# Kernel tuning notes

Measured on AMD Instinct MI355X. Metric: run time of the kernel, lower is better.

## Reference

```python
import jax, jax.numpy as jnp
import numpy as np

EPS = 1e-9
NEG_BIG = -(2.0**32) + 1.0


def dice(x, alpha):
    # BN with center=False, scale=False at inference: moving_mean=0, moving_var=1
    x_norm = x * (1.0 / np.sqrt(1.0 + EPS)).astype(np.float32)
    p = jax.nn.sigmoid(x_norm)
    return alpha * (1.0 - p) * x + p * x


def setup_inputs() -> dict:
    key = jax.random.key(0)
    ks = jax.random.split(key, 12)
    B, T, D = 4096, 200, 128
    U = 128  # gru units == hidden_dim

    def glorot(k, shape):
        fan_in = shape[0]
        return (jax.random.normal(k, shape, dtype=jnp.float32) / np.sqrt(fan_in)).astype(jnp.float32)

    return {
        "interest_seq": jax.random.normal(ks[0], (B, T, D), dtype=jnp.float32),
        "target_emb": jax.random.normal(ks[1], (B, D), dtype=jnp.float32),
        "seq_length": jax.random.randint(ks[2], (B, 1), 0, T, dtype=jnp.int32),
        "W_att1": glorot(ks[3], (4 * D, 64)),
        "alpha1": jnp.zeros((64,), jnp.float32),
        "W_att2": glorot(ks[4], (64, 16)),
        "alpha2": jnp.zeros((16,), jnp.float32),
        "W_att3": glorot(ks[5], (16, 1)),
        "W_u": glorot(ks[6], (D + U, U)),
        "W_r": glorot(ks[7], (D + U, U)),
        "W_c": glorot(ks[8], (D + U, U)),
    }


def reference(interest_seq, target_emb, seq_length, W_att1, alpha1, W_att2, alpha2, W_att3, W_u, W_r, W_c):
    B, T, D = interest_seq.shape
    U = W_u.shape[1]

    # ---- Attention scores (return_score=True, sigmoid, no weight norm) ----
    q = jnp.broadcast_to(target_emb[:, None, :], (B, T, D))  # [B,T,D]
    k = interest_seq
    att_in = jnp.concatenate([q, k, q - k, q * k], axis=-1)  # [B,T,4D]
    h1 = dice(jnp.einsum('btf,fh->bth', att_in, W_att1), alpha1)
    h2 = dice(jnp.einsum('bth,hg->btg', h1, W_att2), alpha2)
    score = jnp.einsum('btg,go->bto', h2, W_att3)  # [B,T,1]

    valid = jnp.arange(T)[None, :] < seq_length  # [B,T] bool
    vmask = valid.astype(jnp.float32)[:, :, None]
    score = score * vmask + (1.0 - vmask) * NEG_BIG
    att = jax.nn.sigmoid(score)[:, :, 0]  # [B,T]

    # ---- AUGRU scan (return final hidden state) ----
    def step(h, xs):
        x_t, a_t, m_t = xs  # [B,D], [B], [B] bool
        gi = jnp.concatenate([x_t, h], axis=-1)  # [B, D+U]
        u = jax.nn.sigmoid(gi @ W_u)
        r = jax.nn.sigmoid(gi @ W_r)
        c = jnp.tanh(jnp.concatenate([x_t, r * h], axis=-1) @ W_c)
        u_t = u * a_t[:, None]
        h_new = (1.0 - u_t) * h + u_t * c
        h = jnp.where(m_t[:, None], h_new, h)
        return h, None

    xs = (jnp.swapaxes(interest_seq, 0, 1),  # [T,B,D]
          att.T,                              # [T,B]
          valid.T)                            # [T,B]
    h0 = jnp.zeros((B, U), dtype=interest_seq.dtype)
    h_final, _ = jax.lax.scan(step, h0, xs)
    return h_final
```

## Files before the change

kernel.cpp:

```cpp
#include <hip/hip_runtime.h>
#include <math.h>

typedef __bf16 bf16;
typedef __bf16 bf16x8 __attribute__((ext_vector_type(8)));
typedef float  f32x4  __attribute__((ext_vector_type(4)));

#define MFMA16(a,b,c) __builtin_amdgcn_mfma_f32_16x16x32_bf16((a),(b),(c),0,0,0)

#define B_SZ 4096
#define T_SZ 200
#define D_SZ 128
#define U_SZ 128
#define ACHUNK 4
#define AROWS 16
#define ATTB 8

__device__ __forceinline__ float frcp_(float x) { return __builtin_amdgcn_rcpf(x); }
__device__ __forceinline__ float fsig(float x)  { return frcp_(1.0f + __expf(-x)); }
__device__ __forceinline__ float ftanh_(float x){ return 1.0f - 2.0f * frcp_(1.0f + __expf(2.0f * x)); }
__device__ __forceinline__ float dicef(float x, float alpha) {
    float p = fsig(x);
    return alpha * (1.0f - p) * x + p * x;
}
__device__ __forceinline__ void bar_lgkm() {
    asm volatile("s_waitcnt lgkmcnt(0)\n\ts_barrier" ::: "memory");
}

__global__ __launch_bounds__(256) void prep_kernel(
    const float* __restrict__ Q,
    const float* __restrict__ W1,
    const float* __restrict__ W2,
    float* __restrict__ BIAS,
    bf16*  __restrict__ W1P,
    bf16*  __restrict__ W2T)
{
    const int tid = threadIdx.x;
    if (blockIdx.x == 256) {
        #pragma unroll 4
        for (int it = 0; it < 64; ++it) {
            int idx = it * 256 + tid;
            int k = idx >> 6;
            int n = idx & 63;
            float v;
            if (k < 128) v = W1[(128 + k) * 64 + n] - W1[(256 + k) * 64 + n];
            else         v = W1[(384 + (k - 128)) * 64 + n];
            W1P[n * 256 + k] = (bf16)v;
        }
        #pragma unroll
        for (int it = 0; it < 4; ++it) {
            int idx = it * 256 + tid; int k = idx >> 4; int n = idx & 15;
            W2T[n * 64 + k] = (bf16)W2[k * 16 + n];
        }
        return;
    }
    const int b0   = blockIdx.x * 16;
    const int lane = tid & 63;
    const int w    = tid >> 6;
    const int quad = lane >> 4;
    const int l15  = lane & 15;

    bf16x8 a[4];
    #pragma unroll
    for (int kk = 0; kk < 4; ++kk) {
        const float* p = Q + (long)(b0 + l15) * D_SZ + kk * 32 + quad * 8;
        float4 x0 = ((const float4*)p)[0];
        float4 x1 = ((const float4*)p)[1];
        float xv[8] = {x0.x, x0.y, x0.z, x0.w, x1.x, x1.y, x1.z, x1.w};
        #pragma unroll
        for (int j = 0; j < 8; ++j) a[kk][j] = (bf16)xv[j];
    }
    const int n = w * 16 + l15;
    f32x4 acc = {};
    #pragma unroll
    for (int kk = 0; kk < 4; ++kk) {
        bf16x8 bf;
        #pragma unroll
        for (int j = 0; j < 8; ++j) {
            int k = kk * 32 + quad * 8 + j;
            bf[j] = (bf16)(W1[k * 64 + n] + W1[(256 + k) * 64 + n]);
        }
        acc = MFMA16(a[kk], bf, acc);
    }
    #pragma unroll
    for (int i = 0; i < 4; ++i)
        BIAS[(long)(b0 + quad * 4 + i) * 64 + n] = acc[i];
}

__global__ __launch_bounds__(256) void attn_kernel(
    const float* __restrict__ X,
    const float* __restrict__ Q,
    const int*   __restrict__ LEN,
    const float* __restrict__ A1,
    const float* __restrict__ A2,
    const float* __restrict__ W3,
    const float* __restrict__ BIAS,
    const bf16*  __restrict__ W1P,
    const bf16*  __restrict__ W2T,
    float* __restrict__ ATT)
{
    __shared__ bf16  H1s[64][72];
    __shared__ float qf[ATTB][128];
    __shared__ float bias_s[ATTB][64];
    __shared__ float al1[64];
    __shared__ float al2[16];
    __shared__ float w3s[16];
    __shared__ int   lens[ATTB];

    const int tid  = threadIdx.x;
    const int lane = tid & 63;
    const int w    = tid >> 6;
    const int quad = lane >> 4;
    const int l15  = lane & 15;
    const long b0  = (long)blockIdx.x * ATTB;

    for (int i = tid; i < ATTB * 128; i += 256) qf[i >> 7][i & 127] = Q[b0 * 128 + i];
    for (int i = tid; i < ATTB * 64;  i += 256) bias_s[i >> 6][i & 63] = BIAS[b0 * 64 + i];
    if (tid < 64) al1[tid] = A1[tid];
    if (tid < 16) { al2[tid] = A2[tid]; w3s[tid] = W3[tid]; }
    if (tid < ATTB) lens[tid] = LEN[b0 + tid];

    bf16x8 b1[4][8];
    #pragma unroll
    for (int nt = 0; nt < 4; ++nt)
        #pragma unroll
        for (int kk = 0; kk < 8; ++kk)
            b1[nt][kk] = *(const bf16x8*)(W1P + (nt * 16 + l15) * 256 + kk * 32 + quad * 8);
    bf16x8 b2[2];
    #pragma unroll
    for (int kk = 0; kk < 2; ++kk)
        b2[kk] = *(const bf16x8*)(W2T + l15 * 64 + kk * 32 + quad * 8);
    __syncthreads();

    const int NT = 13 * ATTB;
    float4 fb[8];
    auto issue = [&](int g) {
        int bi = g / 13, mt = g - bi * 13;
        int row = mt * 16 + l15;
        int rc  = row < T_SZ ? row : (T_SZ - 1);
        const float* xp = X + ((b0 + bi) * T_SZ + rc) * D_SZ;
        #pragma unroll
        for (int kc = 0; kc < 4; ++kc) {
            const float* p = xp + kc * 32 + quad * 8;
            fb[kc * 2]     = ((const float4*)p)[0];
            fb[kc * 2 + 1] = ((const float4*)p)[1];
        }
    };
    auto convert = [&](int g, bf16x8* axd, bf16x8* aqd) {
        int bi = g / 13;
        #pragma unroll
        for (int kc = 0; kc < 4; ++kc) {
            float4 xa = fb[kc * 2], xb = fb[kc * 2 + 1];
            float xv[8] = {xa.x, xa.y, xa.z, xa.w, xb.x, xb.y, xb.z, xb.w};
            const float* qp = &qf[bi][kc * 32 + quad * 8];
            #pragma unroll
            for (int j = 0; j < 8; ++j) {
                axd[kc][j] = (bf16)xv[j];
                aqd[kc][j] = (bf16)(xv[j] * qp[j]);
            }
        }
    };

    bf16x8 axc[4], aqc[4];
    issue(w);
    convert(w, axc, aqc);

    for (int g = w; g < NT; g += 4) {
        const int gn = g + 4;
        if (gn < NT) issue(gn);

        f32x4 acc[4] = {};
        #pragma unroll
        for (int kc = 0; kc < 4; ++kc)
            #pragma unroll
            for (int nt = 0; nt < 4; ++nt) {
                acc[nt] = MFMA16(axc[kc], b1[nt][kc],     acc[nt]);
                acc[nt] = MFMA16(aqc[kc], b1[nt][kc + 4], acc[nt]);
            }

        const int bi = g / 13, mt = g - bi * 13;
        const int m0 = mt * 16;
        #pragma unroll
        for (int nt = 0; nt < 4; ++nt) {
            int n = nt * 16 + l15;
            float bia = bias_s[bi][n]; float al = al1[n];
            #pragma unroll
            for (int i = 0; i < 4; ++i) {
                float v = acc[nt][i] + bia;
                H1s[w * 16 + quad * 4 + i][n] = (bf16)dicef(v, al);
            }
        }
        f32x4 acc2 = {};
        #pragma unroll
        for (int kk = 0; kk < 2; ++kk) {
            bf16x8 a2 = *(const bf16x8*)&H1s[w * 16 + l15][kk * 32 + quad * 8];
            acc2 = MFMA16(a2, b2[kk], acc2);
        }
        {
            float al = al2[l15]; float w3 = w3s[l15];
            float s[4];
            #pragma unroll
            for (int i = 0; i < 4; ++i) s[i] = dicef(acc2[i], al) * w3;
            #pragma unroll
            for (int i = 0; i < 4; ++i) {
                s[i] += __shfl_xor(s[i], 1, 64);
                s[i] += __shfl_xor(s[i], 2, 64);
                s[i] += __shfl_xor(s[i], 4, 64);
                s[i] += __shfl_xor(s[i], 8, 64);
            }
            if (l15 == 0) {
                int len = lens[bi];
                #pragma unroll
                for (int i = 0; i < 4; ++i) {
                    int t = m0 + quad * 4 + i;
                    if (t < T_SZ)
                        ATT[(b0 + bi) * T_SZ + t] = (t < len) ? fsig(s[i]) : 0.0f;
                }
            }
        }
        if (gn < NT) convert(gn, axc, aqc);
    }
}

__global__ __launch_bounds__(512) void augru_kernel(
    const float* __restrict__ X,
    const float* __restrict__ ATT,
    const float* __restrict__ WU,
    const float* __restrict__ WR,
    const float* __restrict__ WC,
    float* __restrict__ OUT)
{
    __shared__ bf16  Xs[2][ACHUNK][16][136];
    __shared__ float As[2][ACHUNK][16];
    __shared__ bf16  Hb[16][136];
    __shared__ bf16  RHb[16][136];

    const int tid  = threadIdx.x;
    const int lane = tid & 63;
    const int w    = tid >> 6;
    const int quad = lane >> 4;
    const int l15  = lane & 15;
    const int b0   = blockIdx.x * AROWS;
    const int n    = w * 16 + l15;

    for (int i = tid; i < 16 * 136; i += 512) { ((bf16*)Hb)[i] = (bf16)0.f; ((bf16*)RHb)[i] = (bf16)0.f; }

    bf16x8 Wf[3][2][4];
    {
        const float* Wg[3] = {WU, WR, WC};
        #pragma unroll
        for (int g = 0; g < 3; ++g)
            #pragma unroll
            for (int p = 0; p < 2; ++p)
                #pragma unroll
                for (int kk = 0; kk < 4; ++kk) {
                    #pragma unroll
                    for (int i = 0; i < 8; ++i) {
                        int k = p * 128 + kk * 32 + quad * 8 + i;
                        Wf[g][p][kk][i] = (bf16)Wg[g][k * 128 + n];
                    }
                }
    }

    float h[4] = {0.f, 0.f, 0.f, 0.f};

    float4 pf[4];
    float  pa = 0.f;
    auto issue_loads = [&](int c) {
        #pragma unroll
        for (int it = 0; it < 4; ++it) {
            int gidx = it * 512 + tid;
            int c4 = gidx & 31;
            int pair = gidx >> 5;
            int r = pair & 15;
            int s = pair >> 4;
            pf[it] = *(const float4*)(X + ((long)(b0 + r) * T_SZ + (c * ACHUNK + s)) * D_SZ + c4 * 4);
        }
        if (tid < ACHUNK * 16) {
            int r = tid & 15; int s = tid >> 4;
            pa = ATT[(long)(b0 + r) * T_SZ + c * ACHUNK + s];
        }
    };
    auto commit_part = [&](int buf, int it) {
        int gidx = it * 512 + tid;
        int c4 = gidx & 31;
        int pair = gidx >> 5;
        int r = pair & 15;
        int s = pair >> 4;
        bf16* dst = &Xs[buf][s][r][c4 * 4];
        float4 v = pf[it];
        dst[0] = (bf16)v.x; dst[1] = (bf16)v.y; dst[2] = (bf16)v.z; dst[3] = (bf16)v.w;
        if (it == 0 && tid < ACHUNK * 16) {
            int r2 = tid & 15; int s2 = tid >> 4;
            As[buf][s2][r2] = pa;
        }
    };
    auto xparts = [&](int buf, int s, f32x4& pr_, f32x4& pu_, f32x4& pc_) {
        f32x4 r0 = {}, u0 = {}, c0 = {};
        #pragma unroll
        for (int kk = 0; kk < 4; ++kk) {
            bf16x8 ax = *(const bf16x8*)&Xs[buf][s][l15][kk * 32 + quad * 8];
            r0 = MFMA16(ax, Wf[1][0][kk], r0);
            u0 = MFMA16(ax, Wf[0][0][kk], u0);
            c0 = MFMA16(ax, Wf[2][0][kk], c0);
        }
        pr_ = r0; pu_ = u0; pc_ = c0;
    };

    issue_loads(0);
    #pragma unroll
    for (int it = 0; it < 4; ++it) commit_part(0, it);
    bar_lgkm();

    f32x4 pr, pu, pc;
    xparts(0, 0, pr, pu, pc);

    const int NCH = T_SZ / ACHUNK;
    for (int c = 0; c < NCH; ++c) {
        const int buf = c & 1;
        if (c + 1 < NCH) issue_loads(c + 1);

        #pragma unroll
        for (int s = 0; s < ACHUNK; ++s) {
            bf16x8 ah[4];
            #pragma unroll
            for (int kk = 0; kk < 4; ++kk)
                ah[kk] = *(const bf16x8*)&Hb[l15][kk * 32 + quad * 8];
            #pragma unroll
            for (int kk = 0; kk < 4; ++kk) {
                pr = MFMA16(ah[kk], Wf[1][1][kk], pr);
                pu = MFMA16(ah[kk], Wf[0][1][kk], pu);
            }
            float uu[4];
            #pragma unroll
            for (int i = 0; i < 4; ++i) {
                float rr = fsig(pr[i]);
                RHb[quad * 4 + i][n] = (bf16)(rr * h[i]);
                uu[i] = fsig(pu[i]);
            }
            bar_lgkm();
            bf16x8 ar[4];
            #pragma unroll
            for (int kk = 0; kk < 4; ++kk)
                ar[kk] = *(const bf16x8*)&RHb[l15][kk * 32 + quad * 8];
            #pragma unroll
            for (int kk = 0; kk < 4; ++kk)
                pc = MFMA16(ar[kk], Wf[2][1][kk], pc);
            f32x4 prN, puN, pcN;
            if (s + 1 < ACHUNK) xparts(buf, s + 1, prN, puN, pcN);
            #pragma unroll
            for (int i = 0; i < 4; ++i) {
                float a  = As[buf][s][quad * 4 + i];
                float cg = ftanh_(pc[i]);
                float ut = uu[i] * a;
                float hn = (1.f - ut) * h[i] + ut * cg;
                h[i] = hn;
                Hb[quad * 4 + i][n] = (bf16)hn;
            }
            if (c + 1 < NCH) commit_part(buf ^ 1, s);
            bar_lgkm();
            if (s + 1 < ACHUNK) { pr = prN; pu = puN; pc = pcN; }
        }
        if (c + 1 < NCH) xparts(buf ^ 1, 0, pr, pu, pc);
    }

    #pragma unroll
    for (int i = 0; i < 4; ++i)
        OUT[(long)(b0 + quad * 4 + i) * U_SZ + n] = h[i];
}

extern "C" void kernel_launch(void* const* d_in, const int* in_sizes, int n_in,
                              void* d_out, int out_size, void* d_ws, size_t ws_size,
                              hipStream_t stream) {
    const float* X   = (const float*)d_in[0];
    const float* Q   = (const float*)d_in[1];
    const int*   LEN = (const int*)d_in[2];
    const float* W1  = (const float*)d_in[3];
    const float* A1  = (const float*)d_in[4];
    const float* W2  = (const float*)d_in[5];
    const float* A2  = (const float*)d_in[6];
    const float* W3  = (const float*)d_in[7];
    const float* WU  = (const float*)d_in[8];
    const float* WR  = (const float*)d_in[9];
    const float* WC  = (const float*)d_in[10];
    float* OUT = (float*)d_out;

    float* ATT  = (float*)d_ws;
    float* BIAS = ATT + (size_t)B_SZ * T_SZ;
    bf16*  W1P  = (bf16*)(BIAS + (size_t)B_SZ * 64);
    bf16*  W2T  = W1P + 64 * 256;

    prep_kernel<<<257, 256, 0, stream>>>(Q, W1, W2, BIAS, W1P, W2T);
    attn_kernel<<<B_SZ / ATTB, 256, 0, stream>>>(X, Q, LEN, A1, A2, W3, BIAS, W1P, W2T, ATT);
    augru_kernel<<<B_SZ / AROWS, 512, 0, stream>>>(X, ATT, WU, WR, WC, OUT);
}
```

Measured before the change: 833.1 us.

## Fuse attention scoring into AUGRU scan kernel to avoid second pass over X

Merges the attention kernel into the AUGRU kernel. X is staged once per chunk into shared memory as bf16, and its product with the query is formed alongside it. Warps 0-3 compute the first attention layer for the next chunk and warps 4-7 compute the final score for the current step, in the slack of the recurrent step. This removes a full second read of the large interest sequence and the ATT round-trip through global memory. In exchange it adds per-step work and shared memory on the latency-bound scan, which can lower occupancy or lengthen the critical path.

```diff
diff --git a/kernel.cpp b/kernel.cpp
--- a/kernel.cpp
+++ b/kernel.cpp
@@ -13,7 +13,6 @@
 #define U_SZ 128
 #define ACHUNK 4
 #define AROWS 16
-#define ATTB 8
 
 __device__ __forceinline__ float frcp_(float x) { return __builtin_amdgcn_rcpf(x); }
 __device__ __forceinline__ float fsig(float x)  { return frcp_(1.0f + __expf(-x)); }
@@ -86,153 +85,31 @@
         BIAS[(long)(b0 + quad * 4 + i) * 64 + n] = acc[i];
 }
 
-__global__ __launch_bounds__(256) void attn_kernel(
+__global__ __launch_bounds__(512) void fused_kernel(
     const float* __restrict__ X,
     const float* __restrict__ Q,
     const int*   __restrict__ LEN,
     const float* __restrict__ A1,
-    const float* __restrict__ A2,
-    const float* __restrict__ W3,
+    const float* __restrict__ A2g,
+    const float* __restrict__ W3g,
     const float* __restrict__ BIAS,
     const bf16*  __restrict__ W1P,
     const bf16*  __restrict__ W2T,
-    float* __restrict__ ATT)
-{
-    __shared__ bf16  H1s[64][72];
-    __shared__ float qf[ATTB][128];
-    __shared__ float bias_s[ATTB][64];
-    __shared__ float al1[64];
-    __shared__ float al2[16];
-    __shared__ float w3s[16];
-    __shared__ int   lens[ATTB];
-
-    const int tid  = threadIdx.x;
-    const int lane = tid & 63;
-    const int w    = tid >> 6;
-    const int quad = lane >> 4;
-    const int l15  = lane & 15;
-    const long b0  = (long)blockIdx.x * ATTB;
-
-    for (int i = tid; i < ATTB * 128; i += 256) qf[i >> 7][i & 127] = Q[b0 * 128 + i];
-    for (int i = tid; i < ATTB * 64;  i += 256) bias_s[i >> 6][i & 63] = BIAS[b0 * 64 + i];
-    if (tid < 64) al1[tid] = A1[tid];
-    if (tid < 16) { al2[tid] = A2[tid]; w3s[tid] = W3[tid]; }
-    if (tid < ATTB) lens[tid] = LEN[b0 + tid];
-
-    bf16x8 b1[4][8];
-    #pragma unroll
-    for (int nt = 0; nt < 4; ++nt)
-        #pragma unroll
-        for (int kk = 0; kk < 8; ++kk)
-            b1[nt][kk] = *(const bf16x8*)(W1P + (nt * 16 + l15) * 256 + kk * 32 + quad * 8);
-    bf16x8 b2[2];
-    #pragma unroll
-    for (int kk = 0; kk < 2; ++kk)
-        b2[kk] = *(const bf16x8*)(W2T + l15 * 64 + kk * 32 + quad * 8);
-    __syncthreads();
-
-    const int NT = 13 * ATTB;
-    float4 fb[8];
-    auto issue = [&](int g) {
-        int bi = g / 13, mt = g - bi * 13;
-        int row = mt * 16 + l15;
-        int rc  = row < T_SZ ? row : (T_SZ - 1);
-        const float* xp = X + ((b0 + bi) * T_SZ + rc) * D_SZ;
-        #pragma unroll
-        for (int kc = 0; kc < 4; ++kc) {
-            const float* p = xp + kc * 32 + quad * 8;
-            fb[kc * 2]     = ((const float4*)p)[0];
-            fb[kc * 2 + 1] = ((const float4*)p)[1];
-        }
-    };
-    auto convert = [&](int g, bf16x8* axd, bf16x8* aqd) {
-        int bi = g / 13;
-        #pragma unroll
-        for (int kc = 0; kc < 4; ++kc) {
-            float4 xa = fb[kc * 2], xb = fb[kc * 2 + 1];
-            float xv[8] = {xa.x, xa.y, xa.z, xa.w, xb.x, xb.y, xb.z, xb.w};
-            const float* qp = &qf[bi][kc * 32 + quad * 8];
-            #pragma unroll
-            for (int j = 0; j < 8; ++j) {
-                axd[kc][j] = (bf16)xv[j];
-                aqd[kc][j] = (bf16)(xv[j] * qp[j]);
-            }
-        }
-    };
-
-    bf16x8 axc[4], aqc[4];
-    issue(w);
-    convert(w, axc, aqc);
-
-    for (int g = w; g < NT; g += 4) {
-        const int gn = g + 4;
-        if (gn < NT) issue(gn);
-
-        f32x4 acc[4] = {};
-        #pragma unroll
-        for (int kc = 0; kc < 4; ++kc)
-            #pragma unroll
-            for (int nt = 0; nt < 4; ++nt) {
-                acc[nt] = MFMA16(axc[kc], b1[nt][kc],     acc[nt]);
-                acc[nt] = MFMA16(aqc[kc], b1[nt][kc + 4], acc[nt]);
-            }
-
-        const int bi = g / 13, mt = g - bi * 13;
-        const int m0 = mt * 16;
-        #pragma unroll
-        for (int nt = 0; nt < 4; ++nt) {
-            int n = nt * 16 + l15;
-            float bia = bias_s[bi][n]; float al = al1[n];
-            #pragma unroll
-            for (int i = 0; i < 4; ++i) {
-                float v = acc[nt][i] + bia;
-                H1s[w * 16 + quad * 4 + i][n] = (bf16)dicef(v, al);
-            }
-        }
-        f32x4 acc2 = {};
-        #pragma unroll
-        for (int kk = 0; kk < 2; ++kk) {
-            bf16x8 a2 = *(const bf16x8*)&H1s[w * 16 + l15][kk * 32 + quad * 8];
-            acc2 = MFMA16(a2, b2[kk], acc2);
-        }
-        {
-            float al = al2[l15]; float w3 = w3s[l15];
-            float s[4];
-            #pragma unroll
-            for (int i = 0; i < 4; ++i) s[i] = dicef(acc2[i], al) * w3;
-            #pragma unroll
-            for (int i = 0; i < 4; ++i) {
-                s[i] += __shfl_xor(s[i], 1, 64);
-                s[i] += __shfl_xor(s[i], 2, 64);
-                s[i] += __shfl_xor(s[i], 4, 64);
-                s[i] += __shfl_xor(s[i], 8, 64);
-            }
-            if (l15 == 0) {
-                int len = lens[bi];
-                #pragma unroll
-                for (int i = 0; i < 4; ++i) {
-                    int t = m0 + quad * 4 + i;
-                    if (t < T_SZ)
-                        ATT[(b0 + bi) * T_SZ + t] = (t < len) ? fsig(s[i]) : 0.0f;
-                }
-            }
-        }
-        if (gn < NT) convert(gn, axc, aqc);
-    }
-}
-
-__global__ __launch_bounds__(512) void augru_kernel(
-    const float* __restrict__ X,
-    const float* __restrict__ ATT,
     const float* __restrict__ WU,
     const float* __restrict__ WR,
     const float* __restrict__ WC,
     float* __restrict__ OUT)
 {
     __shared__ bf16  Xs[2][ACHUNK][16][136];
-    __shared__ float As[2][ACHUNK][16];
+    __shared__ bf16  XQs[ACHUNK][16][136];
+    __shared__ bf16  W1s[64 * 264];
     __shared__ bf16  Hb[16][136];
     __shared__ bf16  RHb[16][136];
+    __shared__ bf16  H1s[ACHUNK * 16 * 72];
+    __shared__ float qf[16 * 132];
+    __shared__ float bias_s[16 * 68];
+    __shared__ float As[ACHUNK * 16];
+    __shared__ int   lens16[16];
 
     const int tid  = threadIdx.x;
     const int lane = tid & 63;
@@ -242,7 +119,28 @@
     const int b0   = blockIdx.x * AROWS;
     const int n    = w * 16 + l15;
 
+    for (int idx = tid; idx < 64 * 32; idx += 512) {
+        int nn = idx >> 5, k8 = idx & 31;
+        *(bf16x8*)&W1s[nn * 264 + k8 * 8] = *(const bf16x8*)(W1P + nn * 256 + k8 * 8);
+    }
+    for (int i = tid; i < 16 * 128; i += 512) {
+        int r = i >> 7, k = i & 127;
+        qf[r * 132 + k] = Q[(long)(b0 + r) * D_SZ + k];
+    }
+    for (int i = tid; i < 16 * 64; i += 512) {
+        int r = i >> 6, c2 = i & 63;
+        bias_s[r * 68 + c2] = BIAS[(long)(b0 + r) * 64 + c2];
+    }
+    if (tid < 16) lens16[tid] = LEN[b0 + tid];
     for (int i = tid; i < 16 * 136; i += 512) { ((bf16*)Hb)[i] = (bf16)0.f; ((bf16*)RHb)[i] = (bf16)0.f; }
+
+    const float al1v = A1[(w & 3) * 16 + l15];
+    const float al2v = A2g[l15];
+    const float w3v  = W3g[l15];
+    bf16x8 b2f[2];
+    #pragma unroll
+    for (int kk = 0; kk < 2; ++kk)
+        b2f[kk] = *(const bf16x8*)(W2T + l15 * 64 + kk * 32 + quad * 8);
 
     bf16x8 Wf[3][2][4];
     {
@@ -264,7 +162,6 @@
     float h[4] = {0.f, 0.f, 0.f, 0.f};
 
     float4 pf[4];
-    float  pa = 0.f;
     auto issue_loads = [&](int c) {
         #pragma unroll
         for (int it = 0; it < 4; ++it) {
@@ -275,48 +172,95 @@
             int s = pair >> 4;
             pf[it] = *(const float4*)(X + ((long)(b0 + r) * T_SZ + (c * ACHUNK + s)) * D_SZ + c4 * 4);
         }
-        if (tid < ACHUNK * 16) {
-            int r = tid & 15; int s = tid >> 4;
-            pa = ATT[(long)(b0 + r) * T_SZ + c * ACHUNK + s];
-        }
-    };
-    auto commit_part = [&](int buf, int it) {
+    };
+    auto commit_part = [&](int bufw, int it) {
         int gidx = it * 512 + tid;
         int c4 = gidx & 31;
         int pair = gidx >> 5;
         int r = pair & 15;
-        int s = pair >> 4;
-        bf16* dst = &Xs[buf][s][r][c4 * 4];
+        int sl = pair >> 4;
         float4 v = pf[it];
-        dst[0] = (bf16)v.x; dst[1] = (bf16)v.y; dst[2] = (bf16)v.z; dst[3] = (bf16)v.w;
-        if (it == 0 && tid < ACHUNK * 16) {
-            int r2 = tid & 15; int s2 = tid >> 4;
-            As[buf][s2][r2] = pa;
-        }
-    };
-    auto xparts = [&](int buf, int s, f32x4& pr_, f32x4& pu_, f32x4& pc_) {
+        float4 qv = *(const float4*)&qf[r * 132 + c4 * 4];
+        bf16* dx = &Xs[bufw][sl][r][c4 * 4];
+        bf16* dq = &XQs[sl][r][c4 * 4];
+        dx[0] = (bf16)v.x; dx[1] = (bf16)v.y; dx[2] = (bf16)v.z; dx[3] = (bf16)v.w;
+        dq[0] = (bf16)(v.x * qv.x); dq[1] = (bf16)(v.y * qv.y);
+        dq[2] = (bf16)(v.z * qv.z); dq[3] = (bf16)(v.w * qv.w);
+    };
+    auto xparts = [&](int bufw, int s, f32x4& pr_, f32x4& pu_, f32x4& pc_) {
         f32x4 r0 = {}, u0 = {}, c0 = {};
         #pragma unroll
         for (int kk = 0; kk < 4; ++kk) {
-            bf16x8 ax = *(const bf16x8*)&Xs[buf][s][l15][kk * 32 + quad * 8];
+            bf16x8 ax = *(const bf16x8*)&Xs[bufw][s][l15][kk * 32 + quad * 8];
             r0 = MFMA16(ax, Wf[1][0][kk], r0);
             u0 = MFMA16(ax, Wf[0][0][kk], u0);
             c0 = MFMA16(ax, Wf[2][0][kk], c0);
         }
         pr_ = r0; pu_ = u0; pc_ = c0;
     };
+    auto h1f = [&](int bufw, int s) {
+        f32x4 acc = {};
+        #pragma unroll
+        for (int kk = 0; kk < 4; ++kk) {
+            bf16x8 ax = *(const bf16x8*)&Xs[bufw][s][l15][kk * 32 + quad * 8];
+            bf16x8 bw = *(const bf16x8*)&W1s[n * 264 + kk * 32 + quad * 8];
+            acc = MFMA16(ax, bw, acc);
+        }
+        #pragma unroll
+        for (int kk = 0; kk < 4; ++kk) {
+            bf16x8 aq = *(const bf16x8*)&XQs[s][l15][kk * 32 + quad * 8];
+            bf16x8 bw = *(const bf16x8*)&W1s[n * 264 + 128 + kk * 32 + quad * 8];
+            acc = MFMA16(aq, bw, acc);
+        }
+        #pragma unroll
+        for (int i = 0; i < 4; ++i) {
+            int row = quad * 4 + i;
+            float v = acc[i] + bias_s[row * 68 + n];
+            H1s[(s * 16 + row) * 72 + n] = (bf16)dicef(v, al1v);
+        }
+    };
+    auto h23f = [&](int s, int cc) {
+        f32x4 acc2 = {};
+        #pragma unroll
+        for (int kk = 0; kk < 2; ++kk) {
+            bf16x8 a2 = *(const bf16x8*)&H1s[(s * 16 + l15) * 72 + kk * 32 + quad * 8];
+            acc2 = MFMA16(a2, b2f[kk], acc2);
+        }
+        float sv[4];
+        #pragma unroll
+        for (int i = 0; i < 4; ++i) sv[i] = dicef(acc2[i], al2v) * w3v;
+        #pragma unroll
+        for (int i = 0; i < 4; ++i) {
+            sv[i] += __shfl_xor(sv[i], 1, 64);
+            sv[i] += __shfl_xor(sv[i], 2, 64);
+            sv[i] += __shfl_xor(sv[i], 4, 64);
+            sv[i] += __shfl_xor(sv[i], 8, 64);
+        }
+        if (l15 == 0) {
+            int t = cc * ACHUNK + s;
+            #pragma unroll
+            for (int i = 0; i < 4; ++i) {
+                int row = quad * 4 + i;
+                As[s * 16 + row] = (t < lens16[row]) ? fsig(sv[i]) : 0.0f;
+            }
+        }
+    };
 
     issue_loads(0);
+    __syncthreads();
     #pragma unroll
     for (int it = 0; it < 4; ++it) commit_part(0, it);
     bar_lgkm();
+    if (w < 4) { h1f(0, 0); h1f(0, 1); h1f(0, 2); h1f(0, 3); }
+    bar_lgkm();
 
     f32x4 pr, pu, pc;
     xparts(0, 0, pr, pu, pc);
 
     const int NCH = T_SZ / ACHUNK;
     for (int c = 0; c < NCH; ++c) {
-        const int buf = c & 1;
+        const int buf  = c & 1;
+        const int bufN = buf ^ 1;
         if (c + 1 < NCH) issue_loads(c + 1);
 
         #pragma unroll
@@ -337,6 +281,11 @@
                 RHb[quad * 4 + i][n] = (bf16)(rr * h[i]);
                 uu[i] = fsig(pu[i]);
             }
+            if (w >= 4) {
+                if (w == 4 + s) h23f(s, c);
+            } else if (s >= 1 && c + 1 < NCH) {
+                h1f(bufN, s - 1);
+            }
             bar_lgkm();
             bf16x8 ar[4];
             #pragma unroll
@@ -349,18 +298,21 @@
             if (s + 1 < ACHUNK) xparts(buf, s + 1, prN, puN, pcN);
             #pragma unroll
             for (int i = 0; i < 4; ++i) {
-                float a  = As[buf][s][quad * 4 + i];
+                float a  = As[s * 16 + quad * 4 + i];
                 float cg = ftanh_(pc[i]);
                 float ut = uu[i] * a;
                 float hn = (1.f - ut) * h[i] + ut * cg;
                 h[i] = hn;
                 Hb[quad * 4 + i][n] = (bf16)hn;
             }
-            if (c + 1 < NCH) commit_part(buf ^ 1, s);
+            if (c + 1 < NCH) commit_part(bufN, s);
             bar_lgkm();
             if (s + 1 < ACHUNK) { pr = prN; pu = puN; pc = pcN; }
         }
-        if (c + 1 < NCH) xparts(buf ^ 1, 0, pr, pu, pc);
+        if (c + 1 < NCH) {
+            xparts(bufN, 0, pr, pu, pc);
+            if (w < 4) h1f(bufN, 3);
+        }
     }
 
     #pragma unroll
@@ -384,12 +336,11 @@
     const float* WC  = (const float*)d_in[10];
     float* OUT = (float*)d_out;
 
-    float* ATT  = (float*)d_ws;
-    float* BIAS = ATT + (size_t)B_SZ * T_SZ;
+    float* BIAS = (float*)d_ws;
     bf16*  W1P  = (bf16*)(BIAS + (size_t)B_SZ * 64);
     bf16*  W2T  = W1P + 64 * 256;
 
     prep_kernel<<<257, 256, 0, stream>>>(Q, W1, W2, BIAS, W1P, W2T);
-    attn_kernel<<<B_SZ / ATTB, 256, 0, stream>>>(X, Q, LEN, A1, A2, W3, BIAS, W1P, W2T, ATT);
-    augru_kernel<<<B_SZ / AROWS, 512, 0, stream>>>(X, ATT, WU, WR, WC, OUT);
-}
+    fused_kernel<<<B_SZ / AROWS, 512, 0, stream>>>(X, Q, LEN, A1, A2, W3,
+                                                   BIAS, W1P, W2T, WU, WR, WC, OUT);
+}
```

Measured after the change: 809.8 us. 2.8% less time.
